# Performance work log

Hardware: AMD Instinct MI355X
Metric: run time of the kernel (lower is better)

The kernel has to match this reference:

```python
import jax, jax.numpy as jnp
import numpy as np


def setup_inputs() -> dict:
    key = jax.random.key(0)
    ks = jax.random.split(key, 9)
    B, S, I, H, C = 128, 512, 256, 1024, 10
    s_ih = 1.0 / np.sqrt(H)
    return {
        "x": jax.random.normal(ks[0], (B, S, I), dtype=jnp.float32),
        "h0": jax.random.normal(ks[1], (B, H), dtype=jnp.float32),
        "c0": jax.random.normal(ks[2], (B, H), dtype=jnp.float32),
        "W_ih": jax.random.normal(ks[3], (4 * H, I), dtype=jnp.float32) * s_ih,
        "W_hh": jax.random.normal(ks[4], (4 * H, H), dtype=jnp.float32) * s_ih,
        "b_ih": jax.random.normal(ks[5], (4 * H,), dtype=jnp.float32) * s_ih,
        "b_hh": jax.random.normal(ks[6], (4 * H,), dtype=jnp.float32) * s_ih,
        "W_out": jax.random.normal(ks[7], (C, H), dtype=jnp.float32) * s_ih,
        "b_out": jax.random.normal(ks[8], (C,), dtype=jnp.float32) * s_ih,
    }


def reference(x, h0, c0, W_ih, W_hh, b_ih, b_hh, W_out, b_out):
    H = h0.shape[-1]
    # Precompute input projections for all timesteps in one big GEMM: [S, B, 4H]
    x_t = jnp.transpose(x, (1, 0, 2))  # (S, B, I)
    x_proj = jnp.einsum("sbi,gi->sbg", x_t, W_ih) + b_ih + b_hh

    def step(carry, xp):
        h, c = carry
        gates = xp + h @ W_hh.T  # (B, 4H)
        i, f, g, o = jnp.split(gates, 4, axis=-1)  # torch LSTMCell gate order
        i = jax.nn.sigmoid(i)
        f = jax.nn.sigmoid(f)
        g = jnp.tanh(g)
        o = jax.nn.sigmoid(o)
        c_new = f * c + i * g
        h_new = o * jnp.tanh(c_new)
        return (h_new, c_new), None

    (h_last, _), _ = jax.lax.scan(step, (h0, c0), x_proj)
    return h_last @ W_out.T + b_out  # (B, num_classes)
```

## Files before the change

kernel.cpp:

```cpp
#include <hip/hip_runtime.h>
#include <hip/hip_bf16.h>


#define LSTM_H 1024
#define LSTM_I 256
#define LSTM_S 512
#define LSTM_B 128

typedef float  f32x4  __attribute__((ext_vector_type(4)));
typedef short  bf16x8 __attribute__((ext_vector_type(8)));

static __device__ __forceinline__ unsigned short f2bf(float f) {
    unsigned int u = __float_as_uint(f);
    u += 0x7fffu + ((u >> 16) & 1u);
    return (unsigned short)(u >> 16);
}
static __device__ __forceinline__ float bf2f(unsigned short s) {
    return __uint_as_float(((unsigned int)s) << 16);
}
static __device__ __forceinline__ float sigm(float x) {
    return 1.f / (1.f + __expf(-x));
}
static __device__ __forceinline__ float tanh_fast(float x) {
    return 2.f / (1.f + __expf(-2.f * x)) - 1.f;
}

#define ALOAD64(p)     __hip_atomic_load((const unsigned long long*)(p), __ATOMIC_RELAXED, __HIP_MEMORY_SCOPE_SYSTEM)
#define ASTORE32(p, v) __hip_atomic_store((unsigned int*)(p), (v), __ATOMIC_RELAXED, __HIP_MEMORY_SCOPE_SYSTEM)

__global__ void init_h(const float* __restrict__ h0, unsigned short* hbuf0) {
    int i = blockIdx.x * blockDim.x + threadIdx.x;
    if (i < LSTM_B * LSTM_H / 2) {
        unsigned int packed = (unsigned int)f2bf(h0[2 * i]) |
                              ((unsigned int)f2bf(h0[2 * i + 1]) << 16);
        ASTORE32(((unsigned int*)hbuf0) + i, packed);
    }
}

__global__ __launch_bounds__(512, 2) void lstm_persist(
    const float* __restrict__ x,
    const float* __restrict__ c0,
    const float* __restrict__ W_ih,
    const float* __restrict__ W_hh,
    const float* __restrict__ b_ih,
    const float* __restrict__ b_hh,
    unsigned short* hbuf0, unsigned short* hbuf1,
    unsigned int* flags )
{
    __shared__ short w_ih[64][264];
    __shared__ float gacc[4][32][68];

    const int tid  = threadIdx.x;
    const int bid  = blockIdx.x;
    const int m    = bid & 3;
    const int n    = bid >> 2;
    const int row0 = m * 32;
    const int col0 = n * 16;

    const int lane = tid & 63;
    const int wid  = tid >> 6;
    const int mw   = wid & 1;
    const int kh   = wid >> 1;
    const int l15  = lane & 15;
    const int slot = lane >> 4;
    const int arow = row0 + mw * 16 + l15;

    for (int i = tid; i < 64 * 64; i += 512) {
        const int c = i >> 6, q = i & 63;
        const int grow = (c >> 4) * LSTM_H + col0 + (c & 15);
        float4 v = *((const float4*)(W_ih + (size_t)grow * LSTM_I) + q);
        short* dst = &w_ih[c][q * 4];
        dst[0] = (short)f2bf(v.x); dst[1] = (short)f2bf(v.y);
        dst[2] = (short)f2bf(v.z); dst[3] = (short)f2bf(v.w);
    }

    bf16x8 bw[8][4];
    #pragma unroll
    for (int kk = 0; kk < 8; ++kk) {
        #pragma unroll
        for (int t = 0; t < 4; ++t) {
            const float* p = W_hh + (size_t)(t * LSTM_H + col0 + l15) * LSTM_H
                           + kh * 256 + kk * 32 + slot * 8;
            float4 a = *(const float4*)p;
            float4 b = *(const float4*)(p + 4);
            union { bf16x8 v; unsigned short e[8]; } u;
            u.e[0] = f2bf(a.x); u.e[1] = f2bf(a.y); u.e[2] = f2bf(a.z); u.e[3] = f2bf(a.w);
            u.e[4] = f2bf(b.x); u.e[5] = f2bf(b.y); u.e[6] = f2bf(b.z); u.e[7] = f2bf(b.w);
            bw[kk][t] = u.v;
        }
    }

    const int crow = tid >> 4;
    const int chc  = tid & 15;
    const int hcol = col0 + chc;
    float cstate = c0[(size_t)(row0 + crow) * LSTM_H + hcol];
    const float bi = b_ih[hcol]                + b_hh[hcol];
    const float bf = b_ih[LSTM_H + hcol]       + b_hh[LSTM_H + hcol];
    const float bg = b_ih[2 * LSTM_H + hcol]   + b_hh[2 * LSTM_H + hcol];
    const float bo = b_ih[3 * LSTM_H + hcol]   + b_hh[3 * LSTM_H + hcol];

    const float* xbase = x + (size_t)arow * (LSTM_S * LSTM_I);

    const unsigned short* hread  = hbuf0;
    unsigned short*       hwrite = hbuf1;

    __syncthreads();

    for (int s = 0; s < LSTM_S; ++s) {
        f32x4 acc[4];
        #pragma unroll
        for (int t = 0; t < 4; ++t) acc[t] = (f32x4){0.f, 0.f, 0.f, 0.f};

        #pragma unroll
        for (int kk = 0; kk < 2; ++kk) {
            const int k0 = kh * 64 + kk * 32 + slot * 8;
            const float* xp = xbase + (size_t)s * LSTM_I + k0;
            float4 xa = *(const float4*)xp;
            float4 xb = *(const float4*)(xp + 4);
            union { bf16x8 v; unsigned short e[8]; } ux;
            ux.e[0] = f2bf(xa.x); ux.e[1] = f2bf(xa.y); ux.e[2] = f2bf(xa.z); ux.e[3] = f2bf(xa.w);
            ux.e[4] = f2bf(xb.x); ux.e[5] = f2bf(xb.y); ux.e[6] = f2bf(xb.z); ux.e[7] = f2bf(xb.w);
            #pragma unroll
            for (int t = 0; t < 4; ++t) {
                bf16x8 bv = *(const bf16x8*)&w_ih[t * 16 + l15][k0];
                acc[t] = __builtin_amdgcn_mfma_f32_16x16x32_bf16(ux.v, bv, acc[t], 0, 0, 0);
            }
        }

        if (wid == 0) {
            const unsigned long long* fp = ((const unsigned long long*)flags) + lane * 2;
            const unsigned g = (unsigned)s;
            int guard = 0;
            for (;;) {
                unsigned long long q0 = ALOAD64(fp);
                unsigned long long q1 = ALOAD64(fp + 1);
                int ok = ((unsigned)q0 >= g) & ((unsigned)(q0 >> 32) >= g) &
                         ((unsigned)q1 >= g) & ((unsigned)(q1 >> 32) >= g);
                if (__all(ok)) break;
                __builtin_amdgcn_s_sleep(2);
                if (++guard > (1 << 18)) break;
            }
        }
        __syncthreads();
        asm volatile("" ::: "memory");

        const unsigned short* hr = hread + (size_t)arow * LSTM_H + kh * 256 + slot * 8;
        unsigned long long aq[8][2];
        #pragma unroll
        for (int kk = 0; kk < 8; ++kk) {
            aq[kk][0] = ALOAD64(hr + kk * 32);
            aq[kk][1] = ALOAD64(hr + kk * 32 + 4);
        }
        #pragma unroll
        for (int kk = 0; kk < 8; ++kk) {
            union { bf16x8 v; unsigned long long q[2]; } ua;
            ua.q[0] = aq[kk][0]; ua.q[1] = aq[kk][1];
            #pragma unroll
            for (int t = 0; t < 4; ++t)
                acc[t] = __builtin_amdgcn_mfma_f32_16x16x32_bf16(ua.v, bw[kk][t], acc[t], 0, 0, 0);
        }

        #pragma unroll
        for (int t = 0; t < 4; ++t)
            #pragma unroll
            for (int r = 0; r < 4; ++r)
                gacc[kh][mw * 16 + slot * 4 + r][t * 16 + l15] = acc[t][r];
        __syncthreads();

        {
            float gi = gacc[0][crow][chc]      + gacc[1][crow][chc]      +
                       gacc[2][crow][chc]      + gacc[3][crow][chc]      + bi;
            float gf = gacc[0][crow][16 + chc] + gacc[1][crow][16 + chc] +
                       gacc[2][crow][16 + chc] + gacc[3][crow][16 + chc] + bf;
            float gg = gacc[0][crow][32 + chc] + gacc[1][crow][32 + chc] +
                       gacc[2][crow][32 + chc] + gacc[3][crow][32 + chc] + bg;
            float go = gacc[0][crow][48 + chc] + gacc[1][crow][48 + chc] +
                       gacc[2][crow][48 + chc] + gacc[3][crow][48 + chc] + bo;
            float iv = sigm(gi), fv = sigm(gf), gv = tanh_fast(gg), ov = sigm(go);
            cstate = fv * cstate + iv * gv;
            float hnew = ov * tanh_fast(cstate);
            unsigned short hb = f2bf(hnew);
            int pv = __shfl_down((int)hb, 1);
            if ((chc & 1) == 0) {
                unsigned int packed = (unsigned int)hb | ((unsigned int)pv << 16);
                ASTORE32(hwrite + (size_t)(row0 + crow) * LSTM_H + col0 + chc, packed);
            }
        }

        __syncthreads();
        if (tid == 0) ASTORE32(&flags[bid], (unsigned)(s + 1));

        const unsigned short* t2 = hread;
        hread = hwrite; hwrite = (unsigned short*)t2;
    }
}

__global__ void out_proj(const unsigned short* __restrict__ hbuf,
                         const float* __restrict__ W_out,
                         const float* __restrict__ b_out,
                         float* __restrict__ out) {
    const int gtid = blockIdx.x * 256 + threadIdx.x;
    const int wid  = gtid >> 6;
    const int lane = gtid & 63;
    const int b = wid / 10, c = wid % 10;
    const unsigned short* hr = hbuf + (size_t)b * LSTM_H;
    const float* wr = W_out + (size_t)c * LSTM_H;
    float sum = 0.f;
    #pragma unroll
    for (int k4 = 0; k4 < 4; ++k4) {
        const int kb = (k4 * 64 + lane) * 4;
        unsigned long long q = *(const unsigned long long*)(hr + kb);
        #pragma unroll
        for (int j = 0; j < 4; ++j)
            sum += bf2f((unsigned short)(q >> (16 * j))) * wr[kb + j];
    }
    #pragma unroll
    for (int off = 32; off > 0; off >>= 1) sum += __shfl_down(sum, off);
    if (lane == 0) out[b * 10 + c] = sum + b_out[c];
}

extern "C" void kernel_launch(void* const* d_in, const int* in_sizes, int n_in,
                              void* d_out, int out_size, void* d_ws, size_t ws_size,
                              hipStream_t stream) {
    const float* x     = (const float*)d_in[0];
    const float* h0    = (const float*)d_in[1];
    const float* c0    = (const float*)d_in[2];
    const float* W_ih  = (const float*)d_in[3];
    const float* W_hh  = (const float*)d_in[4];
    const float* b_ih  = (const float*)d_in[5];
    const float* b_hh  = (const float*)d_in[6];
    const float* W_out = (const float*)d_in[7];
    const float* b_out = (const float*)d_in[8];
    float* out = (float*)d_out;

    unsigned short* hbuf0 = (unsigned short*)d_ws;
    unsigned short* hbuf1 = hbuf0 + LSTM_B * LSTM_H;
    unsigned int*   flags = (unsigned int*)((char*)d_ws + 2 * (size_t)LSTM_B * LSTM_H * 2);

    hipMemsetAsync(flags, 0, 1024, stream);
    hipLaunchKernelGGL(init_h, dim3(256), dim3(256), 0, stream, h0, hbuf0);
    hipLaunchKernelGGL(lstm_persist, dim3(256), dim3(512), 0, stream,
                       x, c0, W_ih, W_hh, b_ih, b_hh, hbuf0, hbuf1, flags);
    hipLaunchKernelGGL(out_proj, dim3(320), dim3(256), 0, stream, hbuf0, W_out, b_out, out);
}
```

Before: 3.258 ms.

## Sync only within row-group and use agent-scope acquire/release flags

Replaces the all-block flag barrier with a wait on only the 64 blocks of the same batch-row group (indexed by m), since each group needs only its own rows of h. Atomics move from system to agent scope with an explicit release store and acquire fence, and h is read with plain vector loads instead of per-64-bit atomic loads. The sleep in the spin loop is removed. This shrinks the per-timestep dependency set and memory-ordering overhead, but correctness now relies on blocks being partitioned by m exactly as the flags index assumes.

```diff
diff --git a/kernel.cpp b/kernel.cpp
--- a/kernel.cpp
+++ b/kernel.cpp
@@ -25,8 +25,8 @@
     return 2.f / (1.f + __expf(-2.f * x)) - 1.f;
 }
 
-#define ALOAD64(p)     __hip_atomic_load((const unsigned long long*)(p), __ATOMIC_RELAXED, __HIP_MEMORY_SCOPE_SYSTEM)
-#define ASTORE32(p, v) __hip_atomic_store((unsigned int*)(p), (v), __ATOMIC_RELAXED, __HIP_MEMORY_SCOPE_SYSTEM)
+#define ALOAD32(p)     __hip_atomic_load((const unsigned int*)(p), __ATOMIC_RELAXED, __HIP_MEMORY_SCOPE_AGENT)
+#define ASTORE32(p, v) __hip_atomic_store((unsigned int*)(p), (v), __ATOMIC_RELAXED, __HIP_MEMORY_SCOPE_AGENT)
 
 __global__ void init_h(const float* __restrict__ h0, unsigned short* hbuf0) {
     int i = blockIdx.x * blockDim.x + threadIdx.x;
@@ -100,6 +100,7 @@
     const float bo = b_ih[3 * LSTM_H + hcol]   + b_hh[3 * LSTM_H + hcol];
 
     const float* xbase = x + (size_t)arow * (LSTM_S * LSTM_I);
+    unsigned int* gflags = flags + m * 64;
 
     const unsigned short* hread  = hbuf0;
     unsigned short*       hwrite = hbuf1;
@@ -128,36 +129,25 @@
         }
 
         if (wid == 0) {
-            const unsigned long long* fp = ((const unsigned long long*)flags) + lane * 2;
-            const unsigned g = (unsigned)s;
+            const unsigned int g = (unsigned)s;
             int guard = 0;
-            for (;;) {
-                unsigned long long q0 = ALOAD64(fp);
-                unsigned long long q1 = ALOAD64(fp + 1);
-                int ok = ((unsigned)q0 >= g) & ((unsigned)(q0 >> 32) >= g) &
-                         ((unsigned)q1 >= g) & ((unsigned)(q1 >> 32) >= g);
-                if (__all(ok)) break;
-                __builtin_amdgcn_s_sleep(2);
-                if (++guard > (1 << 18)) break;
+            while (!__all((int)(ALOAD32(gflags + lane) >= g))) {
+                if (++guard > (1 << 20)) break;
             }
+            __builtin_amdgcn_fence(__ATOMIC_ACQUIRE, "agent");
         }
         __syncthreads();
-        asm volatile("" ::: "memory");
 
         const unsigned short* hr = hread + (size_t)arow * LSTM_H + kh * 256 + slot * 8;
-        unsigned long long aq[8][2];
+        bf16x8 ah[8];
+        #pragma unroll
+        for (int kk = 0; kk < 8; ++kk)
+            ah[kk] = *(const bf16x8*)(hr + kk * 32);
         #pragma unroll
         for (int kk = 0; kk < 8; ++kk) {
-            aq[kk][0] = ALOAD64(hr + kk * 32);
-            aq[kk][1] = ALOAD64(hr + kk * 32 + 4);
-        }
-        #pragma unroll
-        for (int kk = 0; kk < 8; ++kk) {
-            union { bf16x8 v; unsigned long long q[2]; } ua;
-            ua.q[0] = aq[kk][0]; ua.q[1] = aq[kk][1];
             #pragma unroll
             for (int t = 0; t < 4; ++t)
-                acc[t] = __builtin_amdgcn_mfma_f32_16x16x32_bf16(ua.v, bw[kk][t], acc[t], 0, 0, 0);
+                acc[t] = __builtin_amdgcn_mfma_f32_16x16x32_bf16(ah[kk], bw[kk][t], acc[t], 0, 0, 0);
         }
 
         #pragma unroll
@@ -188,7 +178,9 @@
         }
 
         __syncthreads();
-        if (tid == 0) ASTORE32(&flags[bid], (unsigned)(s + 1));
+        if (tid == 0)
+            __hip_atomic_store(&flags[m * 64 + n], (unsigned)(s + 1),
+                               __ATOMIC_RELEASE, __HIP_MEMORY_SCOPE_AGENT);
 
         const unsigned short* t2 = hread;
         hread = hwrite; hwrite = (unsigned short*)t2;
```

After: 5.021 ms. 1.54x slower.
